# Optimization experiments

Measured on AMD Instinct MI355X. Metric: run time of the kernel, lower is better.

## Reference

```python
import jax, jax.numpy as jnp
import numpy as np

TOP_K = 2  # num_experts_per_tok


def setup_inputs() -> dict:
    key = jax.random.key(0)
    k1, k2 = jax.random.split(key)
    hidden_states = jax.random.normal(k1, (4, 4096, 4096), dtype=jnp.float32)
    # nn.Linear(hidden_size, num_experts, bias=False) weight: [num_experts, hidden]
    W = jax.random.normal(k2, (8, 4096), dtype=jnp.float32) * (1.0 / np.sqrt(4096))
    return {"hidden_states": hidden_states, "W": W}


def reference(hidden_states, W):
    B, S, H = hidden_states.shape
    x = hidden_states.reshape(-1, H)  # [N, H]
    # router logits: Linear without bias -> x @ W^T  [N, E]
    router_logits = jnp.einsum('nh,eh->ne', x, W)
    router_probs = jax.nn.softmax(router_logits, axis=-1)
    # top-k over probabilities (ordering identical to top-k over logits)
    routing_weights, selected_experts = jax.lax.top_k(router_probs, TOP_K)
    # normalize_router_prob_before_dropping=False -> softmax over gathered logits
    gathered_logits = jnp.take_along_axis(router_logits, selected_experts, axis=-1)
    routing_weights = jax.nn.softmax(gathered_logits, axis=-1)
    return routing_weights, selected_experts, router_logits
```

## Files before the change

### kernel.cpp

```cpp
#include <hip/hip_runtime.h>
#include <math.h>

namespace {

constexpr int H_DIM = 4096;
constexpr int NE    = 8;
constexpr int TPB   = 16;
constexpr int NW    = 8;
constexpr int HPW   = 512;

__global__ __launch_bounds__(512, 4)
void router_kernel(const float* __restrict__ x, const float* __restrict__ W,
                   float* __restrict__ out, int ntok) {
    const int tid  = threadIdx.x;
    const int wave = tid >> 6;
    const int lane = tid & 63;

    float4 wr[NE][2];
    #pragma unroll
    for (int e = 0; e < NE; ++e) {
        const float4* Wrow = (const float4*)(W + e * H_DIM + wave * HPW);
        #pragma unroll
        for (int j = 0; j < 2; ++j) wr[e][j] = Wrow[j * 64 + lane];
    }

    __shared__ float part[TPB][NW][NE];

    int tok0 = (int)blockIdx.x * TPB;
    if (tok0 + TPB > ntok) tok0 = ntok - TPB;

    const float* xbase = x + (size_t)tok0 * H_DIM + wave * HPW;

    float4 xv[2], xn[2];
    {
        const float4* xr = (const float4*)xbase;
        #pragma unroll
        for (int j = 0; j < 2; ++j) xv[j] = xr[j * 64 + lane];
    }

    for (int t = 0; t < TPB; ++t) {
        if (t + 1 < TPB) {
            const float4* xrn = (const float4*)(xbase + (size_t)(t + 1) * H_DIM);
            #pragma unroll
            for (int j = 0; j < 2; ++j) xn[j] = xrn[j * 64 + lane];
        }

        float v[NE];
        #pragma unroll
        for (int e = 0; e < NE; ++e) {
            float a = 0.0f;
            #pragma unroll
            for (int j = 0; j < 2; ++j) {
                a += xv[j].x * wr[e][j].x;
                a += xv[j].y * wr[e][j].y;
                a += xv[j].z * wr[e][j].z;
                a += xv[j].w * wr[e][j].w;
            }
            v[e] = a;
        }

        const bool b0 = (lane & 1) != 0;
        #pragma unroll
        for (int i = 0; i < 4; ++i) {
            float a = b0 ? v[i + 4] : v[i];
            float b = b0 ? v[i]     : v[i + 4];
            v[i] = a + __shfl_xor(b, 1, 64);
        }
        const bool b1 = (lane & 2) != 0;
        #pragma unroll
        for (int i = 0; i < 2; ++i) {
            float a = b1 ? v[i + 2] : v[i];
            float b = b1 ? v[i]     : v[i + 2];
            v[i] = a + __shfl_xor(b, 2, 64);
        }
        const bool b2 = (lane & 4) != 0;
        {
            float a = b2 ? v[1] : v[0];
            float b = b2 ? v[0] : v[1];
            float s = a + __shfl_xor(b, 4, 64);
            s += __shfl_xor(s, 8, 64);
            s += __shfl_xor(s, 16, 64);
            s += __shfl_xor(s, 32, 64);
            if (lane < 8) {
                const int e = ((lane & 1) << 2) | (lane & 2) | ((lane >> 2) & 1);
                part[t][wave][e] = s;
            }
        }

        #pragma unroll
        for (int j = 0; j < 2; ++j) xv[j] = xn[j];
    }

    __syncthreads();

    if (tid < TPB) {
        const int tok = tok0 + tid;
        float lg[NE];
        #pragma unroll
        for (int e = 0; e < NE; ++e) {
            float a = 0.0f;
            #pragma unroll
            for (int w = 0; w < NW; ++w) a += part[tid][w][e];
            lg[e] = a;
        }

        float* out_w = out;
        float* out_s = out + (size_t)ntok * 2;
        float* out_l = out + (size_t)ntok * 4;

        float4* lp = (float4*)(out_l + (size_t)tok * 8);
        lp[0] = make_float4(lg[0], lg[1], lg[2], lg[3]);
        lp[1] = make_float4(lg[4], lg[5], lg[6], lg[7]);

        int e0 = 0; float m0 = lg[0];
        #pragma unroll
        for (int e = 1; e < NE; ++e) { if (lg[e] > m0) { m0 = lg[e]; e0 = e; } }
        int e1 = -1; float m1 = -INFINITY;
        #pragma unroll
        for (int e = 0; e < NE; ++e) { if (e != e0 && lg[e] > m1) { m1 = lg[e]; e1 = e; } }

        const float d = expf(m1 - m0);
        const float s = 1.0f / (1.0f + d);
        out_w[(size_t)tok * 2]     = s;
        out_w[(size_t)tok * 2 + 1] = d * s;
        out_s[(size_t)tok * 2]     = (float)e0;
        out_s[(size_t)tok * 2 + 1] = (float)e1;
    }
}

}

extern "C" void kernel_launch(void* const* d_in, const int* in_sizes, int n_in,
                              void* d_out, int out_size, void* d_ws, size_t ws_size,
                              hipStream_t stream) {
    const float* x = (const float*)d_in[0];
    const float* W = (const float*)d_in[1];
    float* outp = (float*)d_out;

    const int ntok = in_sizes[0] / H_DIM;
    const int nblk = (ntok + TPB - 1) / TPB;

    router_kernel<<<nblk, 512, 0, stream>>>(x, W, outp, ntok);
}
```

Before: 355.4 us.

## Double waves per block, deepen x prefetch to four tokens with nontemporal loads

```diff
diff --git a/kernel.cpp b/kernel.cpp
--- a/kernel.cpp
+++ b/kernel.cpp
@@ -6,22 +6,24 @@
 constexpr int H_DIM = 4096;
 constexpr int NE    = 8;
 constexpr int TPB   = 16;
-constexpr int NW    = 8;
-constexpr int HPW   = 512;
+constexpr int NW    = 16;
+constexpr int HPW   = 256;
+constexpr int PF    = 4;
 
-__global__ __launch_bounds__(512, 4)
+typedef float f32x4 __attribute__((ext_vector_type(4)));
+
+__global__ __launch_bounds__(1024, 4)
 void router_kernel(const float* __restrict__ x, const float* __restrict__ W,
                    float* __restrict__ out, int ntok) {
     const int tid  = threadIdx.x;
     const int wave = tid >> 6;
     const int lane = tid & 63;
 
-    float4 wr[NE][2];
+    f32x4 wr[NE];
     #pragma unroll
     for (int e = 0; e < NE; ++e) {
-        const float4* Wrow = (const float4*)(W + e * H_DIM + wave * HPW);
-        #pragma unroll
-        for (int j = 0; j < 2; ++j) wr[e][j] = Wrow[j * 64 + lane];
+        const f32x4* Wrow = (const f32x4*)(W + e * H_DIM + wave * HPW);
+        wr[e] = Wrow[lane];
     }
 
     __shared__ float part[TPB][NW][NE];
@@ -31,32 +33,22 @@
 
     const float* xbase = x + (size_t)tok0 * H_DIM + wave * HPW;
 
-    float4 xv[2], xn[2];
-    {
-        const float4* xr = (const float4*)xbase;
-        #pragma unroll
-        for (int j = 0; j < 2; ++j) xv[j] = xr[j * 64 + lane];
-    }
+    f32x4 xb[PF];
+    #pragma unroll
+    for (int p = 0; p < PF; ++p)
+        xb[p] = __builtin_nontemporal_load((const f32x4*)(xbase + (size_t)p * H_DIM) + lane);
 
+    #pragma unroll
     for (int t = 0; t < TPB; ++t) {
-        if (t + 1 < TPB) {
-            const float4* xrn = (const float4*)(xbase + (size_t)(t + 1) * H_DIM);
-            #pragma unroll
-            for (int j = 0; j < 2; ++j) xn[j] = xrn[j * 64 + lane];
-        }
+        const f32x4 xv = xb[t & (PF - 1)];
+        if (t + PF < TPB)
+            xb[t & (PF - 1)] = __builtin_nontemporal_load(
+                (const f32x4*)(xbase + (size_t)(t + PF) * H_DIM) + lane);
 
         float v[NE];
         #pragma unroll
         for (int e = 0; e < NE; ++e) {
-            float a = 0.0f;
-            #pragma unroll
-            for (int j = 0; j < 2; ++j) {
-                a += xv[j].x * wr[e][j].x;
-                a += xv[j].y * wr[e][j].y;
-                a += xv[j].z * wr[e][j].z;
-                a += xv[j].w * wr[e][j].w;
-            }
-            v[e] = a;
+            v[e] = xv.x * wr[e].x + xv.y * wr[e].y + xv.z * wr[e].z + xv.w * wr[e].w;
         }
 
         const bool b0 = (lane & 1) != 0;
@@ -86,9 +78,6 @@
                 part[t][wave][e] = s;
             }
         }
-
-        #pragma unroll
-        for (int j = 0; j < 2; ++j) xv[j] = xn[j];
     }
 
     __syncthreads();
@@ -140,5 +129,5 @@
     const int ntok = in_sizes[0] / H_DIM;
     const int nblk = (ntok + TPB - 1) / TPB;
 
-    router_kernel<<<nblk, 512, 0, stream>>>(x, W, outp, ntok);
+    router_kernel<<<nblk, 1024, 0, stream>>>(x, W, outp, ntok);
 }
```

Measured after the change: 342.7 us. 1.04x faster.
